# Kernel optimization log

Measured on AMD Instinct MI355X. Metric: run time of the kernel, lower is better.

Reference implementation:

```python
import jax, jax.numpy as jnp
import numpy as np

B, N, INP, OUP = 16, 1024, 512, 512
HEADS, DIM_HEAD = 8, 64
INNER = HEADS * DIM_HEAD


def setup_inputs() -> dict:
    key = jax.random.key(0)
    ks = jax.random.split(key, 9)
    return {
        "query": jax.random.normal(ks[0], (B, N, INP), jnp.float32),
        "key": jax.random.normal(ks[1], (B, N, INP), jnp.float32),
        "value": jax.random.normal(ks[2], (B, N, INP), jnp.float32),
        "Wq": jax.random.normal(ks[3], (INP, INNER), jnp.float32) * 0.02,
        "Wk": jax.random.normal(ks[4], (INP, INNER), jnp.float32) * 0.02,
        "Wv": jax.random.normal(ks[5], (INP, INNER), jnp.float32) * 0.02,
        "Wo": jax.random.normal(ks[6], (INNER, OUP), jnp.float32) * 0.02,
        "bo": jax.random.normal(ks[7], (OUP,), jnp.float32) * 0.02,
        "bias_table": jax.random.normal(ks[8], (2 * N - 1, HEADS), jnp.float32) * 0.02,
    }


def reference(query, key, value, Wq, Wk, Wv, Wo, bo, bias_table):
    scale = DIM_HEAD ** -0.5
    split = lambda t: t.reshape(B, N, HEADS, DIM_HEAD).transpose(0, 2, 1, 3)  # b h n d
    q = split(query @ Wq)
    k = split(key @ Wk)
    v = split(value @ Wv)
    dots = jnp.einsum("bhnd,bhmd->bhnm", q, k) * scale
    # relative position index: (i - j) + (N - 1), shape [N, N]
    coords = jnp.arange(N)
    rel_idx = coords[:, None] - coords[None, :] + (N - 1)
    rel_bias = bias_table[rel_idx]            # [N, N, H]
    rel_bias = rel_bias.transpose(2, 0, 1)[None]  # [1, H, N, N]
    attn = jax.nn.softmax(dots + rel_bias, axis=-1)
    out = jnp.einsum("bhnm,bhmd->bhnd", attn, v)
    out = out.transpose(0, 2, 1, 3).reshape(B, N, INNER)
    return out @ Wo + bo
```

## Files before the change

### kernel.cpp

```cpp
#include <hip/hip_runtime.h>
#include <hip/hip_bf16.h>
#include <stdint.h>

#define BB 16
#define SEQ 1024
#define CHN 512
#define NH 8
#define DH 64

typedef short short8 __attribute__((ext_vector_type(8)));
typedef short short4v __attribute__((ext_vector_type(4)));
typedef float f32x4 __attribute__((ext_vector_type(4)));

typedef const __attribute__((address_space(1))) unsigned int* gptr_t;
typedef __attribute__((address_space(3))) unsigned int* lptr_t;

__device__ __forceinline__ void async16(const void* g, void* l) {
    __builtin_amdgcn_global_load_lds((gptr_t)g, (lptr_t)l, 16, 0, 0);
}

__device__ __forceinline__ unsigned short f2bf(float f) {
    unsigned int u = __float_as_uint(f);
    u += 0x7FFF + ((u >> 16) & 1);
    return (unsigned short)(u >> 16);
}

__global__ __launch_bounds__(256) void k_cvt3(const float* __restrict__ a, const float* __restrict__ b,
                                              const float* __restrict__ c,
                                              unsigned short* __restrict__ oa, unsigned short* __restrict__ ob,
                                              unsigned short* __restrict__ oc, int n4) {
    int i = blockIdx.x * 256 + threadIdx.x;
    if (i >= n4) return;
    const float* in = (blockIdx.y == 0) ? a : (blockIdx.y == 1) ? b : c;
    unsigned short* out = (blockIdx.y == 0) ? oa : (blockIdx.y == 1) ? ob : oc;
    float4 v = ((const float4*)in)[i];
    ushort4 o;
    o.x = f2bf(v.x); o.y = f2bf(v.y); o.z = f2bf(v.z); o.w = f2bf(v.w);
    ((ushort4*)out)[i] = o;
}

__global__ __launch_bounds__(256) void k_cvtw4(const float* __restrict__ W0, const float* __restrict__ W1,
                                               const float* __restrict__ W2, const float* __restrict__ W3,
                                               unsigned short* __restrict__ T0, unsigned short* __restrict__ T1,
                                               unsigned short* __restrict__ T2, unsigned short* __restrict__ T3) {
    __shared__ float t[32][33];
    int z = blockIdx.z;
    const float* W = (z == 0) ? W0 : (z == 1) ? W1 : (z == 2) ? W2 : W3;
    unsigned short* Wt = (z == 0) ? T0 : (z == 1) ? T1 : (z == 2) ? T2 : T3;
    int n0 = blockIdx.x * 32, k0 = blockIdx.y * 32;
    int tx = threadIdx.x & 31, ty = threadIdx.x >> 5;
    for (int r = ty; r < 32; r += 8) t[r][tx] = W[(k0 + r) * CHN + n0 + tx];
    __syncthreads();
    for (int r = ty; r < 32; r += 8) Wt[(n0 + r) * CHN + k0 + tx] = f2bf(t[tx][r]);
}

__device__ __forceinline__ void gemm_tile(const unsigned short* __restrict__ A,
                                          const unsigned short* __restrict__ Bt,
                                          int Kdim, int m0, int n0,
                                          f32x4 acc[4][4],
                                          unsigned short* As, unsigned short* Bs) {
    const int tid = threadIdx.x;
    const int lane = tid & 63, wid = tid >> 6;
    const int g = lane >> 4, l16 = lane & 15;
    const int wm = wid >> 1, wn = wid & 1;
    for (int i = 0; i < 4; i++)
        for (int j = 0; j < 4; j++) acc[i][j] = (f32x4){0.f, 0.f, 0.f, 0.f};
    for (int k0 = 0; k0 < Kdim; k0 += 32) {
        for (int c = 0; c < 2; ++c) {
            int seg = c * 256 + tid;
            int row = seg >> 2, ch = seg & 3;
            const unsigned short* ga = A + (size_t)(m0 + row) * Kdim + k0 + ch * 8;
            const unsigned short* gb = Bt + (size_t)(n0 + row) * Kdim + k0 + ch * 8;
            int base = (c * 256 + wid * 64) * 8;
            async16(ga, As + base);
            async16(gb, Bs + base);
        }
        __syncthreads();
        short8 af[4], bfr[4];
        for (int mi = 0; mi < 4; mi++)
            af[mi] = *(const short8*)(As + (wm * 64 + mi * 16 + l16) * 32 + g * 8);
        for (int ni = 0; ni < 4; ni++)
            bfr[ni] = *(const short8*)(Bs + (wn * 64 + ni * 16 + l16) * 32 + g * 8);
        for (int mi = 0; mi < 4; mi++)
            for (int ni = 0; ni < 4; ni++)
                acc[mi][ni] = __builtin_amdgcn_mfma_f32_16x16x32_bf16(af[mi], bfr[ni], acc[mi][ni], 0, 0, 0);
        __syncthreads();
    }
}

__global__ __launch_bounds__(256) void k_gemm_qkv(
    const unsigned short* __restrict__ Xq, const unsigned short* __restrict__ Xk,
    const unsigned short* __restrict__ Xv,
    const unsigned short* __restrict__ Wtq, const unsigned short* __restrict__ Wtk,
    const unsigned short* __restrict__ Wtv,
    unsigned short* __restrict__ Qp, unsigned short* __restrict__ Kp,
    unsigned short* __restrict__ Vtp) {
    __shared__ unsigned short As[128 * 32], Bs[128 * 32];
    int z = blockIdx.z;
    const unsigned short* A = (z == 0) ? Xq : (z == 1) ? Xk : Xv;
    const unsigned short* Bt = (z == 0) ? Wtq : (z == 1) ? Wtk : Wtv;
    int m0 = blockIdx.y * 128, n0 = blockIdx.x * 128;
    f32x4 acc[4][4];
    gemm_tile(A, Bt, CHN, m0, n0, acc, As, Bs);

    const int tid = threadIdx.x, lane = tid & 63, wid = tid >> 6;
    const int g = lane >> 4, l16 = lane & 15;
    const int wm = wid >> 1, wn = wid & 1;
    const float QSC = 0.125f * 1.4426950408889634f;
    if (z < 2) {
        unsigned short* dst = (z == 0) ? Qp : Kp;
        const float sc = (z == 0) ? QSC : 1.0f;
        for (int mi = 0; mi < 4; mi++)
            for (int ni = 0; ni < 4; ni++) {
                int col = n0 + wn * 64 + ni * 16 + l16;
                int h = col >> 6, d = col & 63;
                for (int r = 0; r < 4; r++) {
                    int m = m0 + wm * 64 + mi * 16 + g * 4 + r;
                    int b = m >> 10, i = m & 1023;
                    dst[(((size_t)b * NH + h) * SEQ + i) * DH + d] = f2bf(acc[mi][ni][r] * sc);
                }
            }
    } else {
        for (int mi = 0; mi < 4; mi++)
            for (int ni = 0; ni < 4; ni++) {
                int col = n0 + wn * 64 + ni * 16 + l16;
                int h = col >> 6, d = col & 63;
                int m = m0 + wm * 64 + mi * 16 + g * 4;
                int b = m >> 10, i = m & 1023;
                ushort4 pk;
                pk.x = f2bf(acc[mi][ni][0]); pk.y = f2bf(acc[mi][ni][1]);
                pk.z = f2bf(acc[mi][ni][2]); pk.w = f2bf(acc[mi][ni][3]);
                *(ushort4*)&Vtp[(((size_t)b * NH + h) * DH + d) * SEQ + i] = pk;
            }
    }
}

__global__ __launch_bounds__(256, 4) void k_attn(const unsigned short* __restrict__ Qp,
                                                 const unsigned short* __restrict__ Kp,
                                                 const unsigned short* __restrict__ Vtp,
                                                 const float* __restrict__ bias_table,
                                                 unsigned short* __restrict__ AO) {
    __shared__ unsigned short K_lds[64 * 72];
    __shared__ unsigned short V_lds[64 * 72];
    __shared__ uint2 biasq[1152];
    const int bh = blockIdx.y;
    const int h = bh & (NH - 1);
    const int i0blk = blockIdx.x * 128;
    const int tid = threadIdx.x, lane = tid & 63, w = tid >> 6;
    const int g = lane >> 4, l16 = lane & 15;
    const unsigned short* Qb = Qp + (size_t)bh * SEQ * DH;
    const unsigned short* Kb = Kp + (size_t)bh * SEQ * DH;
    const unsigned short* Vb = Vtp + (size_t)bh * DH * SEQ;

    const float LOG2E = 1.4426950408889634f;
    for (int t = tid; t < 1148; t += 256) {
        const float* bp = bias_table + (size_t)(t + i0blk) * NH + h;
        unsigned int b0 = f2bf(bp[0 * NH] * LOG2E), b1 = f2bf(bp[1 * NH] * LOG2E);
        unsigned int b2 = f2bf(bp[2 * NH] * LOG2E), b3 = f2bf(bp[3 * NH] * LOG2E);
        uint2 q; q.x = (b1 << 16) | b0; q.y = (b3 << 16) | b2;
        biasq[t] = q;
    }

    const int iw = i0blk + w * 32;
    short8 qf[2][2];
    for (int mf = 0; mf < 2; mf++)
        for (int f = 0; f < 2; f++)
            qf[mf][f] = *(const short8*)(Qb + (iw + mf * 16 + l16) * DH + f * 32 + g * 8);

    float lsum[2] = {0.f, 0.f};
    f32x4 acc[2][4];
    for (int mf = 0; mf < 2; mf++)
        for (int db = 0; db < 4; db++) acc[mf][db] = (f32x4){0.f, 0.f, 0.f, 0.f};

    const int r0 = tid >> 3, c0 = tid & 7;
    const int r1 = 32 + (tid >> 3), c1 = tid & 7;
    int4 kr0, kr1, vr0, vr1;
    kr0 = *(const int4*)(Kb + (size_t)r0 * DH + c0 * 8);
    kr1 = *(const int4*)(Kb + (size_t)r1 * DH + c1 * 8);
    vr0 = *(const int4*)(Vb + (size_t)r0 * SEQ + c0 * 8);
    vr1 = *(const int4*)(Vb + (size_t)r1 * SEQ + c1 * 8);

    for (int j0 = 0; j0 < SEQ; j0 += 64) {
        *(int4*)(&K_lds[r0 * 72 + c0 * 8]) = kr0;
        *(int4*)(&K_lds[r1 * 72 + c1 * 8]) = kr1;
        *(int4*)(&V_lds[r0 * 72 + c0 * 8]) = vr0;
        *(int4*)(&V_lds[r1 * 72 + c1 * 8]) = vr1;
        __syncthreads();

        if (j0 + 64 < SEQ) {
            const int jn = j0 + 64;
            kr0 = *(const int4*)(Kb + (size_t)(jn + r0) * DH + c0 * 8);
            kr1 = *(const int4*)(Kb + (size_t)(jn + r1) * DH + c1 * 8);
            vr0 = *(const int4*)(Vb + (size_t)r0 * SEQ + jn + c0 * 8);
            vr1 = *(const int4*)(Vb + (size_t)r1 * SEQ + jn + c1 * 8);
        }

        short8 kfh[4][2];
        for (int jb = 0; jb < 4; jb++)
            for (int f = 0; f < 2; f++)
                kfh[jb][f] = *(const short8*)(&K_lds[(jb * 16 + l16) * 72 + f * 32 + g * 8]);
        short4v vfq[4][4];
        for (int db = 0; db < 4; db++)
            for (int jb = 0; jb < 4; jb++)
                vfq[db][jb] = *(const short4v*)(&V_lds[(db * 16 + l16) * 72 + jb * 16 + g * 4]);

        for (int mf = 0; mf < 2; mf++) {
            const int bb0 = (w * 32 + mf * 16 + l16 + 1023) - j0 - g * 4;
            for (int jb = 0; jb < 4; jb++) {
                const int bb = bb0 - jb * 16;
                const uint2 bq = biasq[bb - 3];
                f32x4 s4 = {__uint_as_float(bq.y & 0xffff0000u),
                            __uint_as_float(bq.y << 16),
                            __uint_as_float(bq.x & 0xffff0000u),
                            __uint_as_float(bq.x << 16)};
                s4 = __builtin_amdgcn_mfma_f32_16x16x32_bf16(kfh[jb][0], qf[mf][0], s4, 0, 0, 0);
                s4 = __builtin_amdgcn_mfma_f32_16x16x32_bf16(kfh[jb][1], qf[mf][1], s4, 0, 0, 0);
                float p0 = __builtin_amdgcn_exp2f(s4[0]);
                float p1 = __builtin_amdgcn_exp2f(s4[1]);
                float p2 = __builtin_amdgcn_exp2f(s4[2]);
                float p3 = __builtin_amdgcn_exp2f(s4[3]);
                lsum[mf] += (p0 + p1) + (p2 + p3);
                uint2 pkd;
                pkd.x = (unsigned int)f2bf(p0) | ((unsigned int)f2bf(p1) << 16);
                pkd.y = (unsigned int)f2bf(p2) | ((unsigned int)f2bf(p3) << 16);
                short4v pk = __builtin_bit_cast(short4v, pkd);
                for (int db = 0; db < 4; db++)
                    acc[mf][db] = __builtin_amdgcn_mfma_f32_16x16x16bf16_1k(
                        vfq[db][jb], pk, acc[mf][db], 0, 0, 0);
            }
        }
        __syncthreads();
    }

    float inv[2];
    for (int mf = 0; mf < 2; mf++) {
        float v = lsum[mf];
        v += __shfl_xor(v, 16, 64);
        v += __shfl_xor(v, 32, 64);
        inv[mf] = 1.0f / v;
    }

    const int b = bh >> 3;
    for (int mf = 0; mf < 2; mf++) {
        const int i = iw + mf * 16 + l16;
        for (int db = 0; db < 4; db++) {
            ushort4 o;
            o.x = f2bf(acc[mf][db][0] * inv[mf]);
            o.y = f2bf(acc[mf][db][1] * inv[mf]);
            o.z = f2bf(acc[mf][db][2] * inv[mf]);
            o.w = f2bf(acc[mf][db][3] * inv[mf]);
            *(ushort4*)&AO[((size_t)b * SEQ + i) * CHN + h * DH + db * 16 + g * 4] = o;
        }
    }
}

__global__ __launch_bounds__(256) void k_gemm_out(const unsigned short* __restrict__ AOb,
                                                  const unsigned short* __restrict__ Wto,
                                                  const float* __restrict__ bo,
                                                  float* __restrict__ out) {
    __shared__ unsigned short As[128 * 32], Bs[128 * 32];
    int m0 = blockIdx.y * 128, n0 = blockIdx.x * 128;
    f32x4 acc[4][4];
    gemm_tile(AOb, Wto, CHN, m0, n0, acc, As, Bs);
    const int tid = threadIdx.x, lane = tid & 63, wid = tid >> 6;
    const int g = lane >> 4, l16 = lane & 15;
    const int wm = wid >> 1, wn = wid & 1;
    for (int ni = 0; ni < 4; ni++) {
        int col = n0 + wn * 64 + ni * 16 + l16;
        float bias = bo[col];
        for (int mi = 0; mi < 4; mi++)
            for (int r = 0; r < 4; r++) {
                int m = m0 + wm * 64 + mi * 16 + g * 4 + r;
                out[(size_t)m * CHN + col] = acc[mi][ni][r] + bias;
            }
    }
}

extern "C" void kernel_launch(void* const* d_in, const int* in_sizes, int n_in,
                              void* d_out, int out_size, void* d_ws, size_t ws_size,
                              hipStream_t stream) {
    const float* q_f = (const float*)d_in[0];
    const float* k_f = (const float*)d_in[1];
    const float* v_f = (const float*)d_in[2];
    const float* Wq_f = (const float*)d_in[3];
    const float* Wk_f = (const float*)d_in[4];
    const float* Wv_f = (const float*)d_in[5];
    const float* Wo_f = (const float*)d_in[6];
    const float* bo_f = (const float*)d_in[7];
    const float* bt_f = (const float*)d_in[8];

    char* ws = (char*)d_ws;
    const size_t S_X = (size_t)BB * SEQ * CHN * 2;
    const size_t S_W = (size_t)CHN * CHN * 2;

    unsigned short* Xq = (unsigned short*)(ws);
    unsigned short* Xk = (unsigned short*)(ws + S_X);
    unsigned short* Xv = (unsigned short*)(ws + 2 * S_X);
    unsigned short* Wtq = (unsigned short*)(ws + 3 * S_X);
    unsigned short* Wtk = (unsigned short*)(ws + 3 * S_X + S_W);
    unsigned short* Wtv = (unsigned short*)(ws + 3 * S_X + 2 * S_W);
    unsigned short* Wto = (unsigned short*)(ws + 3 * S_X + 3 * S_W);
    unsigned short* Qp = (unsigned short*)(ws + 3 * S_X + 4 * S_W);
    unsigned short* Kp = (unsigned short*)(ws + 4 * S_X + 4 * S_W);
    unsigned short* Vtp = (unsigned short*)(ws + 5 * S_X + 4 * S_W);
    unsigned short* AO = Xq;

    const int n4 = BB * SEQ * CHN / 4;
    k_cvt3<<<dim3(n4 / 256, 3), 256, 0, stream>>>(q_f, k_f, v_f, Xq, Xk, Xv, n4);
    k_cvtw4<<<dim3(16, 16, 4), 256, 0, stream>>>(Wq_f, Wk_f, Wv_f, Wo_f, Wtq, Wtk, Wtv, Wto);

    k_gemm_qkv<<<dim3(CHN / 128, BB * SEQ / 128, 3), 256, 0, stream>>>(
        Xq, Xk, Xv, Wtq, Wtk, Wtv, Qp, Kp, Vtp);

    k_attn<<<dim3(SEQ / 128, BB * NH), 256, 0, stream>>>(Qp, Kp, Vtp, bt_f, AO);

    k_gemm_out<<<dim3(CHN / 128, BB * SEQ / 128), 256, 0, stream>>>(
        AO, Wto, bo_f, (float*)d_out);
}
```

Before: 170.1 us.

## Fuse fp32-to-bf16 input conversion into QKV GEMM and widen attention blocks

Removes the separate activation conversion kernel. The QKV GEMM now loads fp32 inputs directly, converts them to bf16 in registers and writes them to LDS, which avoids writing and re-reading a bf16 copy of all three inputs. The attention kernel moves to 512 threads per block, with each wave handling 16 query rows instead of 32 and loading K/V fragments inside the loop. This lowers register pressure so more waves can be resident, at the cost of more LDS fragment reloads per unit of work. The A-operand load in the GEMM becomes synchronous rather than asynchronous, which could expose more memory latency.

```diff
diff --git a/kernel.cpp b/kernel.cpp
--- a/kernel.cpp
+++ b/kernel.cpp
@@ -23,20 +23,6 @@
     unsigned int u = __float_as_uint(f);
     u += 0x7FFF + ((u >> 16) & 1);
     return (unsigned short)(u >> 16);
-}
-
-__global__ __launch_bounds__(256) void k_cvt3(const float* __restrict__ a, const float* __restrict__ b,
-                                              const float* __restrict__ c,
-                                              unsigned short* __restrict__ oa, unsigned short* __restrict__ ob,
-                                              unsigned short* __restrict__ oc, int n4) {
-    int i = blockIdx.x * 256 + threadIdx.x;
-    if (i >= n4) return;
-    const float* in = (blockIdx.y == 0) ? a : (blockIdx.y == 1) ? b : c;
-    unsigned short* out = (blockIdx.y == 0) ? oa : (blockIdx.y == 1) ? ob : oc;
-    float4 v = ((const float4*)in)[i];
-    ushort4 o;
-    o.x = f2bf(v.x); o.y = f2bf(v.y); o.z = f2bf(v.z); o.w = f2bf(v.w);
-    ((ushort4*)out)[i] = o;
 }
 
 __global__ __launch_bounds__(256) void k_cvtw4(const float* __restrict__ W0, const float* __restrict__ W1,
@@ -54,58 +40,59 @@
     for (int r = ty; r < 32; r += 8) Wt[(n0 + r) * CHN + k0 + tx] = f2bf(t[tx][r]);
 }
 
-__device__ __forceinline__ void gemm_tile(const unsigned short* __restrict__ A,
-                                          const unsigned short* __restrict__ Bt,
-                                          int Kdim, int m0, int n0,
-                                          f32x4 acc[4][4],
-                                          unsigned short* As, unsigned short* Bs) {
-    const int tid = threadIdx.x;
-    const int lane = tid & 63, wid = tid >> 6;
-    const int g = lane >> 4, l16 = lane & 15;
-    const int wm = wid >> 1, wn = wid & 1;
-    for (int i = 0; i < 4; i++)
-        for (int j = 0; j < 4; j++) acc[i][j] = (f32x4){0.f, 0.f, 0.f, 0.f};
-    for (int k0 = 0; k0 < Kdim; k0 += 32) {
-        for (int c = 0; c < 2; ++c) {
-            int seg = c * 256 + tid;
-            int row = seg >> 2, ch = seg & 3;
-            const unsigned short* ga = A + (size_t)(m0 + row) * Kdim + k0 + ch * 8;
-            const unsigned short* gb = Bt + (size_t)(n0 + row) * Kdim + k0 + ch * 8;
-            int base = (c * 256 + wid * 64) * 8;
-            async16(ga, As + base);
-            async16(gb, Bs + base);
-        }
-        __syncthreads();
-        short8 af[4], bfr[4];
-        for (int mi = 0; mi < 4; mi++)
-            af[mi] = *(const short8*)(As + (wm * 64 + mi * 16 + l16) * 32 + g * 8);
-        for (int ni = 0; ni < 4; ni++)
-            bfr[ni] = *(const short8*)(Bs + (wn * 64 + ni * 16 + l16) * 32 + g * 8);
-        for (int mi = 0; mi < 4; mi++)
-            for (int ni = 0; ni < 4; ni++)
-                acc[mi][ni] = __builtin_amdgcn_mfma_f32_16x16x32_bf16(af[mi], bfr[ni], acc[mi][ni], 0, 0, 0);
-        __syncthreads();
-    }
-}
-
 __global__ __launch_bounds__(256) void k_gemm_qkv(
-    const unsigned short* __restrict__ Xq, const unsigned short* __restrict__ Xk,
-    const unsigned short* __restrict__ Xv,
+    const float* __restrict__ Xq, const float* __restrict__ Xk,
+    const float* __restrict__ Xv,
     const unsigned short* __restrict__ Wtq, const unsigned short* __restrict__ Wtk,
     const unsigned short* __restrict__ Wtv,
     unsigned short* __restrict__ Qp, unsigned short* __restrict__ Kp,
     unsigned short* __restrict__ Vtp) {
     __shared__ unsigned short As[128 * 32], Bs[128 * 32];
     int z = blockIdx.z;
-    const unsigned short* A = (z == 0) ? Xq : (z == 1) ? Xk : Xv;
+    const float* A = (z == 0) ? Xq : (z == 1) ? Xk : Xv;
     const unsigned short* Bt = (z == 0) ? Wtq : (z == 1) ? Wtk : Wtv;
     int m0 = blockIdx.y * 128, n0 = blockIdx.x * 128;
-    f32x4 acc[4][4];
-    gemm_tile(A, Bt, CHN, m0, n0, acc, As, Bs);
-
-    const int tid = threadIdx.x, lane = tid & 63, wid = tid >> 6;
+
+    const int tid = threadIdx.x;
+    const int lane = tid & 63, wid = tid >> 6;
     const int g = lane >> 4, l16 = lane & 15;
     const int wm = wid >> 1, wn = wid & 1;
+    f32x4 acc[4][4];
+    for (int i = 0; i < 4; i++)
+        for (int j = 0; j < 4; j++) acc[i][j] = (f32x4){0.f, 0.f, 0.f, 0.f};
+
+    for (int k0 = 0; k0 < CHN; k0 += 32) {
+        for (int c = 0; c < 2; ++c) {
+            int seg = c * 256 + tid;
+            int row = seg >> 2, ch = seg & 3;
+            const unsigned short* gb = Bt + (size_t)(n0 + row) * CHN + k0 + ch * 8;
+            async16(gb, Bs + (c * 256 + wid * 64) * 8);
+        }
+        for (int c = 0; c < 2; ++c) {
+            int seg = c * 256 + tid;
+            int row = seg >> 2, ch = seg & 3;
+            const float* ga = A + (size_t)(m0 + row) * CHN + k0 + ch * 8;
+            float4 a0 = *(const float4*)ga;
+            float4 a1 = *(const float4*)(ga + 4);
+            int4 pk;
+            pk.x = (int)((unsigned int)f2bf(a0.x) | ((unsigned int)f2bf(a0.y) << 16));
+            pk.y = (int)((unsigned int)f2bf(a0.z) | ((unsigned int)f2bf(a0.w) << 16));
+            pk.z = (int)((unsigned int)f2bf(a1.x) | ((unsigned int)f2bf(a1.y) << 16));
+            pk.w = (int)((unsigned int)f2bf(a1.z) | ((unsigned int)f2bf(a1.w) << 16));
+            *(int4*)(&As[row * 32 + ch * 8]) = pk;
+        }
+        __syncthreads();
+        short8 af[4], bfr[4];
+        for (int mi = 0; mi < 4; mi++)
+            af[mi] = *(const short8*)(As + (wm * 64 + mi * 16 + l16) * 32 + g * 8);
+        for (int ni = 0; ni < 4; ni++)
+            bfr[ni] = *(const short8*)(Bs + (wn * 64 + ni * 16 + l16) * 32 + g * 8);
+        for (int mi = 0; mi < 4; mi++)
+            for (int ni = 0; ni < 4; ni++)
+                acc[mi][ni] = __builtin_amdgcn_mfma_f32_16x16x32_bf16(af[mi], bfr[ni], acc[mi][ni], 0, 0, 0);
+        __syncthreads();
+    }
+
     const float QSC = 0.125f * 1.4426950408889634f;
     if (z < 2) {
         unsigned short* dst = (z == 0) ? Qp : Kp;
@@ -135,7 +122,7 @@
     }
 }
 
-__global__ __launch_bounds__(256, 4) void k_attn(const unsigned short* __restrict__ Qp,
+__global__ __launch_bounds__(512, 6) void k_attn(const unsigned short* __restrict__ Qp,
                                                  const unsigned short* __restrict__ Kp,
                                                  const unsigned short* __restrict__ Vtp,
                                                  const float* __restrict__ bias_table,
@@ -153,7 +140,7 @@
     const unsigned short* Vb = Vtp + (size_t)bh * DH * SEQ;
 
     const float LOG2E = 1.4426950408889634f;
-    for (int t = tid; t < 1148; t += 256) {
+    for (int t = tid; t < 1148; t += 512) {
         const float* bp = bias_table + (size_t)(t + i0blk) * NH + h;
         unsigned int b0 = f2bf(bp[0 * NH] * LOG2E), b1 = f2bf(bp[1 * NH] * LOG2E);
         unsigned int b2 = f2bf(bp[2 * NH] * LOG2E), b3 = f2bf(bp[3 * NH] * LOG2E);
@@ -161,96 +148,73 @@
         biasq[t] = q;
     }
 
-    const int iw = i0blk + w * 32;
-    short8 qf[2][2];
-    for (int mf = 0; mf < 2; mf++)
-        for (int f = 0; f < 2; f++)
-            qf[mf][f] = *(const short8*)(Qb + (iw + mf * 16 + l16) * DH + f * 32 + g * 8);
-
-    float lsum[2] = {0.f, 0.f};
-    f32x4 acc[2][4];
-    for (int mf = 0; mf < 2; mf++)
-        for (int db = 0; db < 4; db++) acc[mf][db] = (f32x4){0.f, 0.f, 0.f, 0.f};
+    const int iw = i0blk + w * 16;
+    short8 qf[2];
+    for (int f = 0; f < 2; f++)
+        qf[f] = *(const short8*)(Qb + (iw + l16) * DH + f * 32 + g * 8);
+
+    float lsum = 0.f;
+    f32x4 acc[4];
+    for (int db = 0; db < 4; db++) acc[db] = (f32x4){0.f, 0.f, 0.f, 0.f};
 
     const int r0 = tid >> 3, c0 = tid & 7;
-    const int r1 = 32 + (tid >> 3), c1 = tid & 7;
-    int4 kr0, kr1, vr0, vr1;
-    kr0 = *(const int4*)(Kb + (size_t)r0 * DH + c0 * 8);
-    kr1 = *(const int4*)(Kb + (size_t)r1 * DH + c1 * 8);
-    vr0 = *(const int4*)(Vb + (size_t)r0 * SEQ + c0 * 8);
-    vr1 = *(const int4*)(Vb + (size_t)r1 * SEQ + c1 * 8);
+    int4 kr = *(const int4*)(Kb + (size_t)r0 * DH + c0 * 8);
+    int4 vr = *(const int4*)(Vb + (size_t)r0 * SEQ + c0 * 8);
 
     for (int j0 = 0; j0 < SEQ; j0 += 64) {
-        *(int4*)(&K_lds[r0 * 72 + c0 * 8]) = kr0;
-        *(int4*)(&K_lds[r1 * 72 + c1 * 8]) = kr1;
-        *(int4*)(&V_lds[r0 * 72 + c0 * 8]) = vr0;
-        *(int4*)(&V_lds[r1 * 72 + c1 * 8]) = vr1;
+        *(int4*)(&K_lds[r0 * 72 + c0 * 8]) = kr;
+        *(int4*)(&V_lds[r0 * 72 + c0 * 8]) = vr;
         __syncthreads();
 
         if (j0 + 64 < SEQ) {
             const int jn = j0 + 64;
-            kr0 = *(const int4*)(Kb + (size_t)(jn + r0) * DH + c0 * 8);
-            kr1 = *(const int4*)(Kb + (size_t)(jn + r1) * DH + c1 * 8);
-            vr0 = *(const int4*)(Vb + (size_t)r0 * SEQ + jn + c0 * 8);
-            vr1 = *(const int4*)(Vb + (size_t)r1 * SEQ + jn + c1 * 8);
-        }
-
-        short8 kfh[4][2];
-        for (int jb = 0; jb < 4; jb++)
-            for (int f = 0; f < 2; f++)
-                kfh[jb][f] = *(const short8*)(&K_lds[(jb * 16 + l16) * 72 + f * 32 + g * 8]);
-        short4v vfq[4][4];
-        for (int db = 0; db < 4; db++)
-            for (int jb = 0; jb < 4; jb++)
-                vfq[db][jb] = *(const short4v*)(&V_lds[(db * 16 + l16) * 72 + jb * 16 + g * 4]);
-
-        for (int mf = 0; mf < 2; mf++) {
-            const int bb0 = (w * 32 + mf * 16 + l16 + 1023) - j0 - g * 4;
-            for (int jb = 0; jb < 4; jb++) {
-                const int bb = bb0 - jb * 16;
-                const uint2 bq = biasq[bb - 3];
-                f32x4 s4 = {__uint_as_float(bq.y & 0xffff0000u),
-                            __uint_as_float(bq.y << 16),
-                            __uint_as_float(bq.x & 0xffff0000u),
-                            __uint_as_float(bq.x << 16)};
-                s4 = __builtin_amdgcn_mfma_f32_16x16x32_bf16(kfh[jb][0], qf[mf][0], s4, 0, 0, 0);
-                s4 = __builtin_amdgcn_mfma_f32_16x16x32_bf16(kfh[jb][1], qf[mf][1], s4, 0, 0, 0);
-                float p0 = __builtin_amdgcn_exp2f(s4[0]);
-                float p1 = __builtin_amdgcn_exp2f(s4[1]);
-                float p2 = __builtin_amdgcn_exp2f(s4[2]);
-                float p3 = __builtin_amdgcn_exp2f(s4[3]);
-                lsum[mf] += (p0 + p1) + (p2 + p3);
-                uint2 pkd;
-                pkd.x = (unsigned int)f2bf(p0) | ((unsigned int)f2bf(p1) << 16);
-                pkd.y = (unsigned int)f2bf(p2) | ((unsigned int)f2bf(p3) << 16);
-                short4v pk = __builtin_bit_cast(short4v, pkd);
-                for (int db = 0; db < 4; db++)
-                    acc[mf][db] = __builtin_amdgcn_mfma_f32_16x16x16bf16_1k(
-                        vfq[db][jb], pk, acc[mf][db], 0, 0, 0);
+            kr = *(const int4*)(Kb + (size_t)(jn + r0) * DH + c0 * 8);
+            vr = *(const int4*)(Vb + (size_t)r0 * SEQ + jn + c0 * 8);
+        }
+
+        const int bb0 = (w * 16 + l16 + 1023) - j0 - g * 4;
+        for (int jb = 0; jb < 4; jb++) {
+            short8 kf0 = *(const short8*)(&K_lds[(jb * 16 + l16) * 72 + g * 8]);
+            short8 kf1 = *(const short8*)(&K_lds[(jb * 16 + l16) * 72 + 32 + g * 8]);
+            const int bb = bb0 - jb * 16;
+            const uint2 bq = biasq[bb - 3];
+            f32x4 s4 = {__uint_as_float(bq.y & 0xffff0000u),
+                        __uint_as_float(bq.y << 16),
+                        __uint_as_float(bq.x & 0xffff0000u),
+                        __uint_as_float(bq.x << 16)};
+            s4 = __builtin_amdgcn_mfma_f32_16x16x32_bf16(kf0, qf[0], s4, 0, 0, 0);
+            s4 = __builtin_amdgcn_mfma_f32_16x16x32_bf16(kf1, qf[1], s4, 0, 0, 0);
+            float p0 = __builtin_amdgcn_exp2f(s4[0]);
+            float p1 = __builtin_amdgcn_exp2f(s4[1]);
+            float p2 = __builtin_amdgcn_exp2f(s4[2]);
+            float p3 = __builtin_amdgcn_exp2f(s4[3]);
+            lsum += (p0 + p1) + (p2 + p3);
+            uint2 pkd;
+            pkd.x = (unsigned int)f2bf(p0) | ((unsigned int)f2bf(p1) << 16);
+            pkd.y = (unsigned int)f2bf(p2) | ((unsigned int)f2bf(p3) << 16);
+            short4v pk = __builtin_bit_cast(short4v, pkd);
+            for (int db = 0; db < 4; db++) {
+                short4v vf = *(const short4v*)(&V_lds[(db * 16 + l16) * 72 + jb * 16 + g * 4]);
+                acc[db] = __builtin_amdgcn_mfma_f32_16x16x16bf16_1k(vf, pk, acc[db], 0, 0, 0);
             }
         }
         __syncthreads();
     }
 
-    float inv[2];
-    for (int mf = 0; mf < 2; mf++) {
-        float v = lsum[mf];
-        v += __shfl_xor(v, 16, 64);
-        v += __shfl_xor(v, 32, 64);
-        inv[mf] = 1.0f / v;
-    }
+    float v = lsum;
+    v += __shfl_xor(v, 16, 64);
+    v += __shfl_xor(v, 32, 64);
+    const float inv = 1.0f / v;
 
     const int b = bh >> 3;
-    for (int mf = 0; mf < 2; mf++) {
-        const int i = iw + mf * 16 + l16;
-        for (int db = 0; db < 4; db++) {
-            ushort4 o;
-            o.x = f2bf(acc[mf][db][0] * inv[mf]);
-            o.y = f2bf(acc[mf][db][1] * inv[mf]);
-            o.z = f2bf(acc[mf][db][2] * inv[mf]);
-            o.w = f2bf(acc[mf][db][3] * inv[mf]);
-            *(ushort4*)&AO[((size_t)b * SEQ + i) * CHN + h * DH + db * 16 + g * 4] = o;
-        }
+    const int i = iw + l16;
+    for (int db = 0; db < 4; db++) {
+        ushort4 o;
+        o.x = f2bf(acc[db][0] * inv);
+        o.y = f2bf(acc[db][1] * inv);
+        o.z = f2bf(acc[db][2] * inv);
+        o.w = f2bf(acc[db][3] * inv);
+        *(ushort4*)&AO[((size_t)b * SEQ + i) * CHN + h * DH + db * 16 + g * 4] = o;
     }
 }
 
@@ -260,11 +224,34 @@
                                                   float* __restrict__ out) {
     __shared__ unsigned short As[128 * 32], Bs[128 * 32];
     int m0 = blockIdx.y * 128, n0 = blockIdx.x * 128;
-    f32x4 acc[4][4];
-    gemm_tile(AOb, Wto, CHN, m0, n0, acc, As, Bs);
-    const int tid = threadIdx.x, lane = tid & 63, wid = tid >> 6;
+    const int tid = threadIdx.x;
+    const int lane = tid & 63, wid = tid >> 6;
     const int g = lane >> 4, l16 = lane & 15;
     const int wm = wid >> 1, wn = wid & 1;
+    f32x4 acc[4][4];
+    for (int i = 0; i < 4; i++)
+        for (int j = 0; j < 4; j++) acc[i][j] = (f32x4){0.f, 0.f, 0.f, 0.f};
+    for (int k0 = 0; k0 < CHN; k0 += 32) {
+        for (int c = 0; c < 2; ++c) {
+            int seg = c * 256 + tid;
+            int row = seg >> 2, ch = seg & 3;
+            const unsigned short* ga = AOb + (size_t)(m0 + row) * CHN + k0 + ch * 8;
+            const unsigned short* gb = Wto + (size_t)(n0 + row) * CHN + k0 + ch * 8;
+            int base = (c * 256 + wid * 64) * 8;
+            async16(ga, As + base);
+            async16(gb, Bs + base);
+        }
+        __syncthreads();
+        short8 af[4], bfr[4];
+        for (int mi = 0; mi < 4; mi++)
+            af[mi] = *(const short8*)(As + (wm * 64 + mi * 16 + l16) * 32 + g * 8);
+        for (int ni = 0; ni < 4; ni++)
+            bfr[ni] = *(const short8*)(Bs + (wn * 64 + ni * 16 + l16) * 32 + g * 8);
+        for (int mi = 0; mi < 4; mi++)
+            for (int ni = 0; ni < 4; ni++)
+                acc[mi][ni] = __builtin_amdgcn_mfma_f32_16x16x32_bf16(af[mi], bfr[ni], acc[mi][ni], 0, 0, 0);
+        __syncthreads();
+    }
     for (int ni = 0; ni < 4; ni++) {
         int col = n0 + wn * 64 + ni * 16 + l16;
         float bias = bo[col];
@@ -293,26 +280,21 @@
     const size_t S_X = (size_t)BB * SEQ * CHN * 2;
     const size_t S_W = (size_t)CHN * CHN * 2;
 
-    unsigned short* Xq = (unsigned short*)(ws);
-    unsigned short* Xk = (unsigned short*)(ws + S_X);
-    unsigned short* Xv = (unsigned short*)(ws + 2 * S_X);
-    unsigned short* Wtq = (unsigned short*)(ws + 3 * S_X);
-    unsigned short* Wtk = (unsigned short*)(ws + 3 * S_X + S_W);
-    unsigned short* Wtv = (unsigned short*)(ws + 3 * S_X + 2 * S_W);
-    unsigned short* Wto = (unsigned short*)(ws + 3 * S_X + 3 * S_W);
-    unsigned short* Qp = (unsigned short*)(ws + 3 * S_X + 4 * S_W);
-    unsigned short* Kp = (unsigned short*)(ws + 4 * S_X + 4 * S_W);
-    unsigned short* Vtp = (unsigned short*)(ws + 5 * S_X + 4 * S_W);
-    unsigned short* AO = Xq;
-
-    const int n4 = BB * SEQ * CHN / 4;
-    k_cvt3<<<dim3(n4 / 256, 3), 256, 0, stream>>>(q_f, k_f, v_f, Xq, Xk, Xv, n4);
+    unsigned short* AO = (unsigned short*)(ws);
+    unsigned short* Wtq = (unsigned short*)(ws + S_X);
+    unsigned short* Wtk = (unsigned short*)(ws + S_X + S_W);
+    unsigned short* Wtv = (unsigned short*)(ws + S_X + 2 * S_W);
+    unsigned short* Wto = (unsigned short*)(ws + S_X + 3 * S_W);
+    unsigned short* Qp = (unsigned short*)(ws + S_X + 4 * S_W);
+    unsigned short* Kp = (unsigned short*)(ws + 2 * S_X + 4 * S_W);
+    unsigned short* Vtp = (unsigned short*)(ws + 3 * S_X + 4 * S_W);
+
     k_cvtw4<<<dim3(16, 16, 4), 256, 0, stream>>>(Wq_f, Wk_f, Wv_f, Wo_f, Wtq, Wtk, Wtv, Wto);
 
     k_gemm_qkv<<<dim3(CHN / 128, BB * SEQ / 128, 3), 256, 0, stream>>>(
-        Xq, Xk, Xv, Wtq, Wtk, Wtv, Qp, Kp, Vtp);
-
-    k_attn<<<dim3(SEQ / 128, BB * NH), 256, 0, stream>>>(Qp, Kp, Vtp, bt_f, AO);
+        q_f, k_f, v_f, Wtq, Wtk, Wtv, Qp, Kp, Vtp);
+
+    k_attn<<<dim3(SEQ / 128, BB * NH), 512, 0, stream>>>(Qp, Kp, Vtp, bt_f, AO);
 
     k_gemm_out<<<dim3(CHN / 128, BB * SEQ / 128), 256, 0, stream>>>(
         AO, Wto, bo_f, (float*)d_out);
```

After: 167.8 us. About the same (-1.4%).

## Use 8 waves of 16 query rows each in attention kernel to raise occupancy

Applied to the files above, without the earlier changes.

The attention kernel now launches 512 threads per block, and each wave handles 16 query rows instead of 32. K/V tile loading is spread across more threads, so each thread moves one vector per tile instead of two. K and V fragments are read from LDS inside the inner loop instead of being preloaded into registers. This cuts register pressure so more waves can be resident and hide latency. In exchange, each wave reuses the K/V fragments it reads from LDS across fewer query rows, so LDS traffic per unit of compute goes up.

```diff
diff --git a/kernel.cpp b/kernel.cpp
--- a/kernel.cpp
+++ b/kernel.cpp
@@ -135,7 +135,7 @@
     }
 }
 
-__global__ __launch_bounds__(256, 4) void k_attn(const unsigned short* __restrict__ Qp,
+__global__ __launch_bounds__(512, 6) void k_attn(const unsigned short* __restrict__ Qp,
                                                  const unsigned short* __restrict__ Kp,
                                                  const unsigned short* __restrict__ Vtp,
                                                  const float* __restrict__ bias_table,
@@ -153,7 +153,7 @@
     const unsigned short* Vb = Vtp + (size_t)bh * DH * SEQ;
 
     const float LOG2E = 1.4426950408889634f;
-    for (int t = tid; t < 1148; t += 256) {
+    for (int t = tid; t < 1148; t += 512) {
         const float* bp = bias_table + (size_t)(t + i0blk) * NH + h;
         unsigned int b0 = f2bf(bp[0 * NH] * LOG2E), b1 = f2bf(bp[1 * NH] * LOG2E);
         unsigned int b2 = f2bf(bp[2 * NH] * LOG2E), b3 = f2bf(bp[3 * NH] * LOG2E);
@@ -161,96 +161,73 @@
         biasq[t] = q;
     }
 
-    const int iw = i0blk + w * 32;
-    short8 qf[2][2];
-    for (int mf = 0; mf < 2; mf++)
-        for (int f = 0; f < 2; f++)
-            qf[mf][f] = *(const short8*)(Qb + (iw + mf * 16 + l16) * DH + f * 32 + g * 8);
-
-    float lsum[2] = {0.f, 0.f};
-    f32x4 acc[2][4];
-    for (int mf = 0; mf < 2; mf++)
-        for (int db = 0; db < 4; db++) acc[mf][db] = (f32x4){0.f, 0.f, 0.f, 0.f};
+    const int iw = i0blk + w * 16;
+    short8 qf[2];
+    for (int f = 0; f < 2; f++)
+        qf[f] = *(const short8*)(Qb + (iw + l16) * DH + f * 32 + g * 8);
+
+    float lsum = 0.f;
+    f32x4 acc[4];
+    for (int db = 0; db < 4; db++) acc[db] = (f32x4){0.f, 0.f, 0.f, 0.f};
 
     const int r0 = tid >> 3, c0 = tid & 7;
-    const int r1 = 32 + (tid >> 3), c1 = tid & 7;
-    int4 kr0, kr1, vr0, vr1;
-    kr0 = *(const int4*)(Kb + (size_t)r0 * DH + c0 * 8);
-    kr1 = *(const int4*)(Kb + (size_t)r1 * DH + c1 * 8);
-    vr0 = *(const int4*)(Vb + (size_t)r0 * SEQ + c0 * 8);
-    vr1 = *(const int4*)(Vb + (size_t)r1 * SEQ + c1 * 8);
+    int4 kr = *(const int4*)(Kb + (size_t)r0 * DH + c0 * 8);
+    int4 vr = *(const int4*)(Vb + (size_t)r0 * SEQ + c0 * 8);
 
     for (int j0 = 0; j0 < SEQ; j0 += 64) {
-        *(int4*)(&K_lds[r0 * 72 + c0 * 8]) = kr0;
-        *(int4*)(&K_lds[r1 * 72 + c1 * 8]) = kr1;
-        *(int4*)(&V_lds[r0 * 72 + c0 * 8]) = vr0;
-        *(int4*)(&V_lds[r1 * 72 + c1 * 8]) = vr1;
+        *(int4*)(&K_lds[r0 * 72 + c0 * 8]) = kr;
+        *(int4*)(&V_lds[r0 * 72 + c0 * 8]) = vr;
         __syncthreads();
 
         if (j0 + 64 < SEQ) {
             const int jn = j0 + 64;
-            kr0 = *(const int4*)(Kb + (size_t)(jn + r0) * DH + c0 * 8);
-            kr1 = *(const int4*)(Kb + (size_t)(jn + r1) * DH + c1 * 8);
-            vr0 = *(const int4*)(Vb + (size_t)r0 * SEQ + jn + c0 * 8);
-            vr1 = *(const int4*)(Vb + (size_t)r1 * SEQ + jn + c1 * 8);
+            kr = *(const int4*)(Kb + (size_t)(jn + r0) * DH + c0 * 8);
+            vr = *(const int4*)(Vb + (size_t)r0 * SEQ + jn + c0 * 8);
         }
 
-        short8 kfh[4][2];
-        for (int jb = 0; jb < 4; jb++)
-            for (int f = 0; f < 2; f++)
-                kfh[jb][f] = *(const short8*)(&K_lds[(jb * 16 + l16) * 72 + f * 32 + g * 8]);
-        short4v vfq[4][4];
-        for (int db = 0; db < 4; db++)
-            for (int jb = 0; jb < 4; jb++)
-                vfq[db][jb] = *(const short4v*)(&V_lds[(db * 16 + l16) * 72 + jb * 16 + g * 4]);
-
-        for (int mf = 0; mf < 2; mf++) {
-            const int bb0 = (w * 32 + mf * 16 + l16 + 1023) - j0 - g * 4;
-            for (int jb = 0; jb < 4; jb++) {
-                const int bb = bb0 - jb * 16;
-                const uint2 bq = biasq[bb - 3];
-                f32x4 s4 = {__uint_as_float(bq.y & 0xffff0000u),
-                            __uint_as_float(bq.y << 16),
-                            __uint_as_float(bq.x & 0xffff0000u),
-                            __uint_as_float(bq.x << 16)};
-                s4 = __builtin_amdgcn_mfma_f32_16x16x32_bf16(kfh[jb][0], qf[mf][0], s4, 0, 0, 0);
-                s4 = __builtin_amdgcn_mfma_f32_16x16x32_bf16(kfh[jb][1], qf[mf][1], s4, 0, 0, 0);
-                float p0 = __builtin_amdgcn_exp2f(s4[0]);
-                float p1 = __builtin_amdgcn_exp2f(s4[1]);
-                float p2 = __builtin_amdgcn_exp2f(s4[2]);
-                float p3 = __builtin_amdgcn_exp2f(s4[3]);
-                lsum[mf] += (p0 + p1) + (p2 + p3);
-                uint2 pkd;
-                pkd.x = (unsigned int)f2bf(p0) | ((unsigned int)f2bf(p1) << 16);
-                pkd.y = (unsigned int)f2bf(p2) | ((unsigned int)f2bf(p3) << 16);
-                short4v pk = __builtin_bit_cast(short4v, pkd);
-                for (int db = 0; db < 4; db++)
-                    acc[mf][db] = __builtin_amdgcn_mfma_f32_16x16x16bf16_1k(
-                        vfq[db][jb], pk, acc[mf][db], 0, 0, 0);
+        const int bb0 = (w * 16 + l16 + 1023) - j0 - g * 4;
+        for (int jb = 0; jb < 4; jb++) {
+            short8 kf0 = *(const short8*)(&K_lds[(jb * 16 + l16) * 72 + g * 8]);
+            short8 kf1 = *(const short8*)(&K_lds[(jb * 16 + l16) * 72 + 32 + g * 8]);
+            const int bb = bb0 - jb * 16;
+            const uint2 bq = biasq[bb - 3];
+            f32x4 s4 = {__uint_as_float(bq.y & 0xffff0000u),
+                        __uint_as_float(bq.y << 16),
+                        __uint_as_float(bq.x & 0xffff0000u),
+                        __uint_as_float(bq.x << 16)};
+            s4 = __builtin_amdgcn_mfma_f32_16x16x32_bf16(kf0, qf[0], s4, 0, 0, 0);
+            s4 = __builtin_amdgcn_mfma_f32_16x16x32_bf16(kf1, qf[1], s4, 0, 0, 0);
+            float p0 = __builtin_amdgcn_exp2f(s4[0]);
+            float p1 = __builtin_amdgcn_exp2f(s4[1]);
+            float p2 = __builtin_amdgcn_exp2f(s4[2]);
+            float p3 = __builtin_amdgcn_exp2f(s4[3]);
+            lsum += (p0 + p1) + (p2 + p3);
+            uint2 pkd;
+            pkd.x = (unsigned int)f2bf(p0) | ((unsigned int)f2bf(p1) << 16);
+            pkd.y = (unsigned int)f2bf(p2) | ((unsigned int)f2bf(p3) << 16);
+            short4v pk = __builtin_bit_cast(short4v, pkd);
+            for (int db = 0; db < 4; db++) {
+                short4v vf = *(const short4v*)(&V_lds[(db * 16 + l16) * 72 + jb * 16 + g * 4]);
+                acc[db] = __builtin_amdgcn_mfma_f32_16x16x16bf16_1k(vf, pk, acc[db], 0, 0, 0);
             }
         }
         __syncthreads();
     }
 
-    float inv[2];
-    for (int mf = 0; mf < 2; mf++) {
-        float v = lsum[mf];
-        v += __shfl_xor(v, 16, 64);
-        v += __shfl_xor(v, 32, 64);
-        inv[mf] = 1.0f / v;
-    }
+    float v = lsum;
+    v += __shfl_xor(v, 16, 64);
+    v += __shfl_xor(v, 32, 64);
+    const float inv = 1.0f / v;
 
     const int b = bh >> 3;
-    for (int mf = 0; mf < 2; mf++) {
-        const int i = iw + mf * 16 + l16;
-        for (int db = 0; db < 4; db++) {
-            ushort4 o;
-            o.x = f2bf(acc[mf][db][0] * inv[mf]);
-            o.y = f2bf(acc[mf][db][1] * inv[mf]);
-            o.z = f2bf(acc[mf][db][2] * inv[mf]);
-            o.w = f2bf(acc[mf][db][3] * inv[mf]);
-            *(ushort4*)&AO[((size_t)b * SEQ + i) * CHN + h * DH + db * 16 + g * 4] = o;
-        }
+    const int i = iw + l16;
+    for (int db = 0; db < 4; db++) {
+        ushort4 o;
+        o.x = f2bf(acc[db][0] * inv);
+        o.y = f2bf(acc[db][1] * inv);
+        o.z = f2bf(acc[db][2] * inv);
+        o.w = f2bf(acc[db][3] * inv);
+        *(ushort4*)&AO[((size_t)b * SEQ + i) * CHN + h * DH + db * 16 + g * 4] = o;
     }
 }
 
@@ -312,7 +289,7 @@
     k_gemm_qkv<<<dim3(CHN / 128, BB * SEQ / 128, 3), 256, 0, stream>>>(
         Xq, Xk, Xv, Wtq, Wtk, Wtv, Qp, Kp, Vtp);
 
-    k_attn<<<dim3(SEQ / 128, BB * NH), 256, 0, stream>>>(Qp, Kp, Vtp, bt_f, AO);
+    k_attn<<<dim3(SEQ / 128, BB * NH), 512, 0, stream>>>(Qp, Kp, Vtp, bt_f, AO);
 
     k_gemm_out<<<dim3(CHN / 128, BB * SEQ / 128), 256, 0, stream>>>(
         AO, Wto, bo_f, (float*)d_out);
```

New measurement: 168.5 us. No clear change (-1.0%).
